# Kernel optimization log

Hardware: AMD Instinct MI355X
Metric: run time of the kernel (lower is better)

Reference implementation:

```python
import jax, jax.numpy as jnp
import numpy as np

HEADS = 8
EMB = 128

def setup_inputs() -> dict:
    key = jax.random.key(0)
    ks = jax.random.split(key, 5)
    b, t, hin = 4, 128, 1024
    N = 50000
    x = jax.random.normal(ks[0], (b, t, hin), dtype=jnp.float32)
    curiosity_score = jax.random.normal(ks[1], (b, t), dtype=jnp.float32)
    Wq = jax.random.normal(ks[2], (EMB * HEADS, hin), dtype=jnp.float32) * (1.0 / np.sqrt(hin))
    keys = jax.random.normal(ks[3], (N, EMB), dtype=jnp.float32)
    values = jax.random.normal(ks[4], (N,), dtype=jnp.float32)
    return {"x": x, "curiosity_score": curiosity_score, "Wq": Wq, "keys": keys, "values": values}

def reference(x, curiosity_score, Wq, keys, values):
    b, t, hin = x.shape
    h, e = HEADS, EMB
    # query projection (torch Linear, no bias): x @ Wq.T -> (b, t, h*e)
    q = jnp.einsum('bti,oi->bto', x, Wq).reshape(b, t, h, e)
    q = q / (e ** 0.25)
    # scores vs shared offline key bank (N, e); buffer was `heads` identical copies,
    # so broadcasting over h is the same math without materializing repeats.
    scores = jnp.einsum('bthe,ne->bthn', q, keys)          # (b, t, h, N)
    attn = jax.nn.softmax(scores, axis=-1)
    # weighted sum of scalar values; curiosity adds a per-query constant to every
    # value, and since attn rows sum to 1 this equals adding curiosity afterwards.
    out = jnp.einsum('bthn,n->bth', attn, values) + curiosity_score[:, :, None]
    out = out.mean(axis=2)                                  # mean over heads
    return out[:, :, None]                                  # (b, t, 1)
```

## Files before the change

### kernel.cpp

```cpp
#include <hip/hip_runtime.h>

#define NHEADS   8
#define EMB_     128
#define BT_      512
#define HIN_     1024
#define NQ_      4096
#define NKEY_    50000
#define NPAD_    50048
#define NGRP_    3128
#define GPS_     68
#define NSLICES_ 46

#define QSCALE   (0.29730177875068026f * 1.4426950408889634f)

typedef __attribute__((ext_vector_type(8))) short short8v;
typedef __attribute__((ext_vector_type(4))) float float4v;

#if __has_builtin(__builtin_amdgcn_exp2f)
#define EXP2F(x) __builtin_amdgcn_exp2f(x)
#else
#define EXP2F(x) exp2f(x)
#endif

__device__ __forceinline__ short f2bf(float f) {
  unsigned u = __float_as_uint(f);
  u += 0x7fffu + ((u >> 16) & 1u);
  return (short)(u >> 16);
}

#if __has_builtin(__builtin_amdgcn_cvt_pk_bf16_f32)
typedef __attribute__((ext_vector_type(2))) __bf16 bf16x2;
__device__ __forceinline__ unsigned pk2(float a, float b) {
  bf16x2 r = __builtin_amdgcn_cvt_pk_bf16_f32(a, b);
  union { bf16x2 v; unsigned u; } c; c.v = r; return c.u;
}
#else
__device__ __forceinline__ unsigned pk2(float a, float b) {
  return (unsigned)(unsigned short)f2bf(a) | ((unsigned)(unsigned short)f2bf(b) << 16);
}
#endif

__global__ __launch_bounds__(256) void convert_kernel(
    const float* __restrict__ keys, const float* __restrict__ values,
    short* __restrict__ keys_fr, float* __restrict__ vpad) {
#pragma unroll
  for (int j = 0; j < 2; ++j) {
    int g = blockIdx.x * 512 + j * 256 + threadIdx.x;
    int key  = g >> 5;
    int posf = g & 31;
    int lc   = posf >> 1;
    int half = posf & 1;
    union { short4 s; unsigned u[2]; } o;
    if (key < NKEY_) {
      float4 v = ((const float4*)keys)[g];
      o.u[0] = pk2(v.x, v.y);
      o.u[1] = pk2(v.z, v.w);
    } else {
      o.u[0] = 0; o.u[1] = 0;
    }
    int grp = key >> 4, kln = key & 15;
    int ks = lc >> 2, q = lc & 3;
    *(short4*)(keys_fr + ((grp * 4 + ks) * 64 + q * 16 + kln) * 8 + half * 4) = o.s;
    if (posf == 0) vpad[key] = (key < NKEY_) ? values[key] : 0.f;
  }
}

__global__ __launch_bounds__(256) void proj_kernel(
    const float* __restrict__ x, const float* __restrict__ Wq,
    short* __restrict__ qb) {
  const int wave = threadIdx.x >> 6, lane = threadIdx.x & 63;
  const int quad = lane >> 4, ln = lane & 15;
  const int tile = blockIdx.x * 4 + wave;
  const int mt = tile >> 6, ot = tile & 63;
  const float* xrow = x  + (mt * 16 + ln) * HIN_ + quad * 8;
  const float* wrow = Wq + (ot * 16 + ln) * HIN_ + quad * 8;
  float4v d = {0.f, 0.f, 0.f, 0.f};

  float4 xa0 = *(const float4*)(xrow);
  float4 xa1 = *(const float4*)(xrow + 4);
  float4 wa0 = *(const float4*)(wrow);
  float4 wa1 = *(const float4*)(wrow + 4);
  float4 xb0 = *(const float4*)(xrow + 32);
  float4 xb1 = *(const float4*)(xrow + 36);
  float4 wb0 = *(const float4*)(wrow + 32);
  float4 wb1 = *(const float4*)(wrow + 36);

#pragma unroll 1
  for (int k0 = 0; k0 < HIN_; k0 += 64) {
    union { short8v s8; unsigned u[4]; } af, bf;
    af.u[0] = pk2(xa0.x, xa0.y); af.u[1] = pk2(xa0.z, xa0.w);
    af.u[2] = pk2(xa1.x, xa1.y); af.u[3] = pk2(xa1.z, xa1.w);
    bf.u[0] = pk2(wa0.x, wa0.y); bf.u[1] = pk2(wa0.z, wa0.w);
    bf.u[2] = pk2(wa1.x, wa1.y); bf.u[3] = pk2(wa1.z, wa1.w);
    if (k0 + 64 < HIN_) {
      xa0 = *(const float4*)(xrow + k0 + 64);
      xa1 = *(const float4*)(xrow + k0 + 68);
      wa0 = *(const float4*)(wrow + k0 + 64);
      wa1 = *(const float4*)(wrow + k0 + 68);
    }
    d = __builtin_amdgcn_mfma_f32_16x16x32_bf16(af.s8, bf.s8, d, 0, 0, 0);

    af.u[0] = pk2(xb0.x, xb0.y); af.u[1] = pk2(xb0.z, xb0.w);
    af.u[2] = pk2(xb1.x, xb1.y); af.u[3] = pk2(xb1.z, xb1.w);
    bf.u[0] = pk2(wb0.x, wb0.y); bf.u[1] = pk2(wb0.z, wb0.w);
    bf.u[2] = pk2(wb1.x, wb1.y); bf.u[3] = pk2(wb1.z, wb1.w);
    if (k0 + 96 < HIN_) {
      xb0 = *(const float4*)(xrow + k0 + 96);
      xb1 = *(const float4*)(xrow + k0 + 100);
      wb0 = *(const float4*)(wrow + k0 + 96);
      wb1 = *(const float4*)(wrow + k0 + 100);
    }
    d = __builtin_amdgcn_mfma_f32_16x16x32_bf16(af.s8, bf.s8, d, 0, 0, 0);
  }
#pragma unroll
  for (int r2 = 0; r2 < 4; ++r2)
    qb[(mt * 16 + quad * 4 + r2) * HIN_ + ot * 16 + ln] = f2bf(d[r2] * QSCALE);
}

__global__ __launch_bounds__(256) void attn_kernel(
    const short* __restrict__ qb,
    const short* __restrict__ keys_fr,
    const float* __restrict__ vpad,
    float* __restrict__ partials) {
  const int t     = threadIdx.x;
  const int wave  = t >> 6;
  const int lane  = t & 63;
  const int quad  = lane >> 4;
  const int ln    = lane & 15;
  const int qbase = blockIdx.x * 256 + wave * 64;
  const int slice = blockIdx.y;
  const int g0    = slice * GPS_;
  const int g1    = g0 + GPS_;

  short8v a[4][4];
#pragma unroll
  for (int sub = 0; sub < 4; ++sub)
#pragma unroll
    for (int ks = 0; ks < 4; ++ks)
      a[sub][ks] = *(const short8v*)(qb + (qbase + sub * 16 + ln) * EMB_ + ks * 32 + quad * 8);

  float lsum[4][4], asum[4][4];
#pragma unroll
  for (int i = 0; i < 4; ++i)
#pragma unroll
    for (int j = 0; j < 4; ++j) { lsum[i][j] = 0.f; asum[i][j] = 0.f; }

  short8v bA[4], bB[4];
  float vA, vB;
#pragma unroll
  for (int ks = 0; ks < 4; ++ks)
    bA[ks] = *(const short8v*)(keys_fr + ((g0 * 4 + ks) * 64 + lane) * 8);
  vA = vpad[g0 * 16 + ln];
#pragma unroll
  for (int ks = 0; ks < 4; ++ks)
    bB[ks] = *(const short8v*)(keys_fr + (((g0 + 1) * 4 + ks) * 64 + lane) * 8);
  vB = vpad[(g0 + 1) * 16 + ln];

#pragma unroll 1
  for (int g = g0; g < g1; g += 2) {
    {
      float4v d[4];
#pragma unroll
      for (int sub = 0; sub < 4; ++sub) d[sub] = (float4v){0.f, 0.f, 0.f, 0.f};
#pragma unroll
      for (int ks = 0; ks < 4; ++ks)
#pragma unroll
        for (int sub = 0; sub < 4; ++sub)
          d[sub] = __builtin_amdgcn_mfma_f32_16x16x32_bf16(a[sub][ks], bA[ks], d[sub], 0, 0, 0);
      if (g + 2 < g1) {
#pragma unroll
        for (int ks = 0; ks < 4; ++ks)
          bA[ks] = *(const short8v*)(keys_fr + (((g + 2) * 4 + ks) * 64 + lane) * 8);
      }
      float vv = vA;
      if (g + 2 < g1) vA = vpad[(g + 2) * 16 + ln];
#pragma unroll
      for (int sub = 0; sub < 4; ++sub)
#pragma unroll
        for (int r2 = 0; r2 < 4; ++r2) {
          float p = EXP2F(d[sub][r2]);
          lsum[sub][r2] += p;
          asum[sub][r2] = fmaf(p, vv, asum[sub][r2]);
        }
    }
    {
      float4v d[4];
#pragma unroll
      for (int sub = 0; sub < 4; ++sub) d[sub] = (float4v){0.f, 0.f, 0.f, 0.f};
#pragma unroll
      for (int ks = 0; ks < 4; ++ks)
#pragma unroll
        for (int sub = 0; sub < 4; ++sub)
          d[sub] = __builtin_amdgcn_mfma_f32_16x16x32_bf16(a[sub][ks], bB[ks], d[sub], 0, 0, 0);
      if (g + 3 < g1) {
#pragma unroll
        for (int ks = 0; ks < 4; ++ks)
          bB[ks] = *(const short8v*)(keys_fr + (((g + 3) * 4 + ks) * 64 + lane) * 8);
      }
      float vv = vB;
      if (g + 3 < g1) vB = vpad[(g + 3) * 16 + ln];
#pragma unroll
      for (int sub = 0; sub < 4; ++sub)
#pragma unroll
        for (int r2 = 0; r2 < 4; ++r2) {
          float p = EXP2F(d[sub][r2]);
          lsum[sub][r2] += p;
          asum[sub][r2] = fmaf(p, vv, asum[sub][r2]);
        }
    }
  }

#pragma unroll
  for (int sub = 0; sub < 4; ++sub)
#pragma unroll
    for (int r2 = 0; r2 < 4; ++r2) {
      float L = lsum[sub][r2], A = asum[sub][r2];
#pragma unroll
      for (int m = 1; m < 16; m <<= 1) {
        L += __shfl_xor(L, m, 64);
        A += __shfl_xor(A, m, 64);
      }
      if (ln == 0) {
        int q = qbase + sub * 16 + quad * 4 + r2;
        partials[(q * NSLICES_ + slice) * 2 + 0] = L;
        partials[(q * NSLICES_ + slice) * 2 + 1] = A;
      }
    }
}

__global__ __launch_bounds__(256) void finalize_kernel(
    const float* __restrict__ partials, const float* __restrict__ cur,
    float* __restrict__ out) {
  int tid = blockIdx.x * 256 + threadIdx.x;
  int bt = tid >> 3, h = tid & 7;
  int q = bt * NHEADS + h;
  const float4* p = (const float4*)(partials + q * NSLICES_ * 2);
  float sl = 0.f, sa = 0.f;
#pragma unroll
  for (int i = 0; i < NSLICES_ / 2; ++i) {
    float4 v = p[i];
    sl += v.x + v.z;
    sa += v.y + v.w;
  }
  float r = sa / sl;
  r += __shfl_xor(r, 1, 64);
  r += __shfl_xor(r, 2, 64);
  r += __shfl_xor(r, 4, 64);
  if (h == 0) out[bt] = r * (1.f / NHEADS) + cur[bt];
}

extern "C" void kernel_launch(void* const* d_in, const int* in_sizes, int n_in,
                              void* d_out, int out_size, void* d_ws, size_t ws_size,
                              hipStream_t stream) {
  (void)in_sizes; (void)n_in; (void)out_size; (void)ws_size;
  const float* x      = (const float*)d_in[0];
  const float* cur    = (const float*)d_in[1];
  const float* Wq     = (const float*)d_in[2];
  const float* keys   = (const float*)d_in[3];
  const float* values = (const float*)d_in[4];
  float* out = (float*)d_out;

  char* ws = (char*)d_ws;
  short* keys_fr = (short*)(ws);
  float* vpad    = (float*)(ws + 12812288);
  short* qb      = (short*)(ws + 13012480);
  float* part    = (float*)(ws + 14061056);

  hipLaunchKernelGGL(convert_kernel, dim3((NPAD_ * 32) / 512), dim3(256), 0, stream,
                     keys, values, keys_fr, vpad);
  hipLaunchKernelGGL(proj_kernel, dim3(512), dim3(256), 0, stream, x, Wq, qb);
  hipLaunchKernelGGL(attn_kernel, dim3(16, NSLICES_), dim3(256), 0, stream,
                     qb, keys_fr, vpad, part);
  hipLaunchKernelGGL(finalize_kernel, dim3(16), dim3(256), 0, stream, part, cur, out);
}
```

Baseline: 176.3 us.

## Merge key conversion and query projection into one prep launch; raise MFMA priority

```diff
diff --git a/kernel.cpp b/kernel.cpp
--- a/kernel.cpp
+++ b/kernel.cpp
@@ -8,8 +8,12 @@
 #define NKEY_    50000
 #define NPAD_    50048
 #define NGRP_    3128
+#define NGRP_REAL_ 3125
 #define GPS_     68
 #define NSLICES_ 46
+
+#define PROJB_   512
+#define CONVB_   1024
 
 #define QSCALE   (0.29730177875068026f * 1.4426950408889634f)
 
@@ -40,81 +44,80 @@
 }
 #endif
 
-__global__ __launch_bounds__(256) void convert_kernel(
+__global__ __launch_bounds__(256) void prep_kernel(
+    const float* __restrict__ x, const float* __restrict__ Wq,
+    short* __restrict__ qb,
     const float* __restrict__ keys, const float* __restrict__ values,
     short* __restrict__ keys_fr, float* __restrict__ vpad) {
-#pragma unroll
-  for (int j = 0; j < 2; ++j) {
-    int g = blockIdx.x * 512 + j * 256 + threadIdx.x;
-    int key  = g >> 5;
-    int posf = g & 31;
-    int lc   = posf >> 1;
-    int half = posf & 1;
-    union { short4 s; unsigned u[2]; } o;
-    if (key < NKEY_) {
-      float4 v = ((const float4*)keys)[g];
-      o.u[0] = pk2(v.x, v.y);
-      o.u[1] = pk2(v.z, v.w);
-    } else {
-      o.u[0] = 0; o.u[1] = 0;
-    }
-    int grp = key >> 4, kln = key & 15;
-    int ks = lc >> 2, q = lc & 3;
-    *(short4*)(keys_fr + ((grp * 4 + ks) * 64 + q * 16 + kln) * 8 + half * 4) = o.s;
-    if (posf == 0) vpad[key] = (key < NKEY_) ? values[key] : 0.f;
+  if (blockIdx.x < PROJB_) {
+    const int wave = threadIdx.x >> 6, lane = threadIdx.x & 63;
+    const int quad = lane >> 4, ln = lane & 15;
+    const int tile = blockIdx.x * 4 + wave;
+    const int mt = tile >> 6, ot = tile & 63;
+    const float* xrow = x  + (mt * 16 + ln) * HIN_ + quad * 8;
+    const float* wrow = Wq + (ot * 16 + ln) * HIN_ + quad * 8;
+    float4v d = {0.f, 0.f, 0.f, 0.f};
+
+    float4 xa0 = *(const float4*)(xrow);
+    float4 xa1 = *(const float4*)(xrow + 4);
+    float4 wa0 = *(const float4*)(wrow);
+    float4 wa1 = *(const float4*)(wrow + 4);
+    float4 xb0 = *(const float4*)(xrow + 32);
+    float4 xb1 = *(const float4*)(xrow + 36);
+    float4 wb0 = *(const float4*)(wrow + 32);
+    float4 wb1 = *(const float4*)(wrow + 36);
+
+#pragma unroll 1
+    for (int k0 = 0; k0 < HIN_; k0 += 64) {
+      union { short8v s8; unsigned u[4]; } af, bf;
+      af.u[0] = pk2(xa0.x, xa0.y); af.u[1] = pk2(xa0.z, xa0.w);
+      af.u[2] = pk2(xa1.x, xa1.y); af.u[3] = pk2(xa1.z, xa1.w);
+      bf.u[0] = pk2(wa0.x, wa0.y); bf.u[1] = pk2(wa0.z, wa0.w);
+      bf.u[2] = pk2(wa1.x, wa1.y); bf.u[3] = pk2(wa1.z, wa1.w);
+      if (k0 + 64 < HIN_) {
+        xa0 = *(const float4*)(xrow + k0 + 64);
+        xa1 = *(const float4*)(xrow + k0 + 68);
+        wa0 = *(const float4*)(wrow + k0 + 64);
+        wa1 = *(const float4*)(wrow + k0 + 68);
+      }
+      d = __builtin_amdgcn_mfma_f32_16x16x32_bf16(af.s8, bf.s8, d, 0, 0, 0);
+
+      af.u[0] = pk2(xb0.x, xb0.y); af.u[1] = pk2(xb0.z, xb0.w);
+      af.u[2] = pk2(xb1.x, xb1.y); af.u[3] = pk2(xb1.z, xb1.w);
+      bf.u[0] = pk2(wb0.x, wb0.y); bf.u[1] = pk2(wb0.z, wb0.w);
+      bf.u[2] = pk2(wb1.x, wb1.y); bf.u[3] = pk2(wb1.z, wb1.w);
+      if (k0 + 96 < HIN_) {
+        xb0 = *(const float4*)(xrow + k0 + 96);
+        xb1 = *(const float4*)(xrow + k0 + 100);
+        wb0 = *(const float4*)(wrow + k0 + 96);
+        wb1 = *(const float4*)(wrow + k0 + 100);
+      }
+      d = __builtin_amdgcn_mfma_f32_16x16x32_bf16(af.s8, bf.s8, d, 0, 0, 0);
+    }
+#pragma unroll
+    for (int r2 = 0; r2 < 4; ++r2)
+      qb[(mt * 16 + quad * 4 + r2) * HIN_ + ot * 16 + ln] = f2bf(d[r2] * QSCALE);
+  } else {
+    const int cb = blockIdx.x - PROJB_;
+    const int t  = threadIdx.x;
+#pragma unroll 1
+    for (int g = cb; g < NGRP_; g += CONVB_) {
+      if (g < NGRP_REAL_) {
+        const float* src = keys + (g * 16 + (t & 15)) * EMB_ + (t >> 4) * 8;
+        float4 v0 = ((const float4*)src)[0];
+        float4 v1 = ((const float4*)src)[1];
+        union { short8v s8; unsigned u[4]; } o;
+        o.u[0] = pk2(v0.x, v0.y); o.u[1] = pk2(v0.z, v0.w);
+        o.u[2] = pk2(v1.x, v1.y); o.u[3] = pk2(v1.z, v1.w);
+        ((short8v*)keys_fr)[g * 256 + t] = o.s8;
+        if (t < 16) vpad[g * 16 + t] = values[g * 16 + t];
+      } else {
+        short8v z = (short8v)0;
+        ((short8v*)keys_fr)[g * 256 + t] = z;
+        if (t < 16) vpad[g * 16 + t] = 0.f;
+      }
+    }
   }
-}
-
-__global__ __launch_bounds__(256) void proj_kernel(
-    const float* __restrict__ x, const float* __restrict__ Wq,
-    short* __restrict__ qb) {
-  const int wave = threadIdx.x >> 6, lane = threadIdx.x & 63;
-  const int quad = lane >> 4, ln = lane & 15;
-  const int tile = blockIdx.x * 4 + wave;
-  const int mt = tile >> 6, ot = tile & 63;
-  const float* xrow = x  + (mt * 16 + ln) * HIN_ + quad * 8;
-  const float* wrow = Wq + (ot * 16 + ln) * HIN_ + quad * 8;
-  float4v d = {0.f, 0.f, 0.f, 0.f};
-
-  float4 xa0 = *(const float4*)(xrow);
-  float4 xa1 = *(const float4*)(xrow + 4);
-  float4 wa0 = *(const float4*)(wrow);
-  float4 wa1 = *(const float4*)(wrow + 4);
-  float4 xb0 = *(const float4*)(xrow + 32);
-  float4 xb1 = *(const float4*)(xrow + 36);
-  float4 wb0 = *(const float4*)(wrow + 32);
-  float4 wb1 = *(const float4*)(wrow + 36);
-
-#pragma unroll 1
-  for (int k0 = 0; k0 < HIN_; k0 += 64) {
-    union { short8v s8; unsigned u[4]; } af, bf;
-    af.u[0] = pk2(xa0.x, xa0.y); af.u[1] = pk2(xa0.z, xa0.w);
-    af.u[2] = pk2(xa1.x, xa1.y); af.u[3] = pk2(xa1.z, xa1.w);
-    bf.u[0] = pk2(wa0.x, wa0.y); bf.u[1] = pk2(wa0.z, wa0.w);
-    bf.u[2] = pk2(wa1.x, wa1.y); bf.u[3] = pk2(wa1.z, wa1.w);
-    if (k0 + 64 < HIN_) {
-      xa0 = *(const float4*)(xrow + k0 + 64);
-      xa1 = *(const float4*)(xrow + k0 + 68);
-      wa0 = *(const float4*)(wrow + k0 + 64);
-      wa1 = *(const float4*)(wrow + k0 + 68);
-    }
-    d = __builtin_amdgcn_mfma_f32_16x16x32_bf16(af.s8, bf.s8, d, 0, 0, 0);
-
-    af.u[0] = pk2(xb0.x, xb0.y); af.u[1] = pk2(xb0.z, xb0.w);
-    af.u[2] = pk2(xb1.x, xb1.y); af.u[3] = pk2(xb1.z, xb1.w);
-    bf.u[0] = pk2(wb0.x, wb0.y); bf.u[1] = pk2(wb0.z, wb0.w);
-    bf.u[2] = pk2(wb1.x, wb1.y); bf.u[3] = pk2(wb1.z, wb1.w);
-    if (k0 + 96 < HIN_) {
-      xb0 = *(const float4*)(xrow + k0 + 96);
-      xb1 = *(const float4*)(xrow + k0 + 100);
-      wb0 = *(const float4*)(wrow + k0 + 96);
-      wb1 = *(const float4*)(wrow + k0 + 100);
-    }
-    d = __builtin_amdgcn_mfma_f32_16x16x32_bf16(af.s8, bf.s8, d, 0, 0, 0);
-  }
-#pragma unroll
-  for (int r2 = 0; r2 < 4; ++r2)
-    qb[(mt * 16 + quad * 4 + r2) * HIN_ + ot * 16 + ln] = f2bf(d[r2] * QSCALE);
 }
 
 __global__ __launch_bounds__(256) void attn_kernel(
@@ -162,11 +165,13 @@
       float4v d[4];
 #pragma unroll
       for (int sub = 0; sub < 4; ++sub) d[sub] = (float4v){0.f, 0.f, 0.f, 0.f};
+      __builtin_amdgcn_s_setprio(1);
 #pragma unroll
       for (int ks = 0; ks < 4; ++ks)
 #pragma unroll
         for (int sub = 0; sub < 4; ++sub)
           d[sub] = __builtin_amdgcn_mfma_f32_16x16x32_bf16(a[sub][ks], bA[ks], d[sub], 0, 0, 0);
+      __builtin_amdgcn_s_setprio(0);
       if (g + 2 < g1) {
 #pragma unroll
         for (int ks = 0; ks < 4; ++ks)
@@ -187,11 +192,13 @@
       float4v d[4];
 #pragma unroll
       for (int sub = 0; sub < 4; ++sub) d[sub] = (float4v){0.f, 0.f, 0.f, 0.f};
+      __builtin_amdgcn_s_setprio(1);
 #pragma unroll
       for (int ks = 0; ks < 4; ++ks)
 #pragma unroll
         for (int sub = 0; sub < 4; ++sub)
           d[sub] = __builtin_amdgcn_mfma_f32_16x16x32_bf16(a[sub][ks], bB[ks], d[sub], 0, 0, 0);
+      __builtin_amdgcn_s_setprio(0);
       if (g + 3 < g1) {
 #pragma unroll
         for (int ks = 0; ks < 4; ++ks)
@@ -266,9 +273,8 @@
   short* qb      = (short*)(ws + 13012480);
   float* part    = (float*)(ws + 14061056);
 
-  hipLaunchKernelGGL(convert_kernel, dim3((NPAD_ * 32) / 512), dim3(256), 0, stream,
-                     keys, values, keys_fr, vpad);
-  hipLaunchKernelGGL(proj_kernel, dim3(512), dim3(256), 0, stream, x, Wq, qb);
+  hipLaunchKernelGGL(prep_kernel, dim3(PROJB_ + CONVB_), dim3(256), 0, stream,
+                     x, Wq, qb, keys, values, keys_fr, vpad);
   hipLaunchKernelGGL(attn_kernel, dim3(16, NSLICES_), dim3(256), 0, stream,
                      qb, keys_fr, vpad, part);
   hipLaunchKernelGGL(finalize_kernel, dim3(16), dim3(256), 0, stream, part, cur, out);
```

Measured after the change: 173.3 us. No clear change (-1.7%).
